# Optimization experiments

Hardware: AMD Instinct MI355X
Metric: run time of the kernel (lower is better)

The kernel has to match this reference:

```python
import jax, jax.numpy as jnp
import numpy as np

EPS = 1e-5

def _layernorm(x, g, b):
    mu = jnp.mean(x, axis=-1, keepdims=True)
    var = jnp.mean(jnp.square(x - mu), axis=-1, keepdims=True)
    return (x - mu) * jax.lax.rsqrt(var + EPS) * g + b

def setup_inputs() -> dict:
    key = jax.random.key(0)
    ks = jax.random.split(key, 5)
    F_, H, D = 1024, 16, 64
    B, N = 4, 2048
    s = lambda k, shp, fan: jax.random.normal(k, shp, jnp.float32) * (fan ** -0.5)
    return {
        "x": jax.random.normal(ks[0], (B, N, F_), jnp.float32),
        "Wq": s(ks[1], (H * D, F_), F_),
        "Wkv": s(ks[2], (2 * H * D, F_), F_),
        "Wo": s(ks[3], (F_, H * D), H * D),
        "ln_g": jnp.ones((F_,), jnp.float32),
        "ln_b": jnp.zeros((F_,), jnp.float32),
        "lnc_g": jnp.ones((F_,), jnp.float32),
        "lnc_b": jnp.zeros((F_,), jnp.float32),
    }

def reference(x, Wq, Wkv, Wo, ln_g, ln_b, lnc_g, lnc_b):
    H, D = 16, 64
    scale = D ** -0.5
    skip = x
    xn = _layernorm(x, ln_g, ln_b)          # query path norm
    cn = _layernorm(x, lnc_g, lnc_b)        # context (self) norm
    B, N, _ = x.shape
    q = jnp.einsum('bnf,ef->bne', xn, Wq)   # [B,N,H*D]
    kv = jnp.einsum('bnf,ef->bne', cn, Wkv) # [B,N,2*H*D]
    k, v = jnp.split(kv, 2, axis=-1)
    tohd = lambda t: t.reshape(B, N, H, D).transpose(0, 2, 1, 3)  # b h n d
    q, k, v = tohd(q), tohd(k), tohd(v)
    sim = jnp.einsum('bhnd,bhmd->bhnm', q, k) * scale
    attn = jax.nn.softmax(sim, axis=-1)
    out = jnp.einsum('bhnm,bhmd->bhnd', attn, v)
    out = out.transpose(0, 2, 1, 3).reshape(B, N, H * D)
    out = jnp.einsum('bne,fe->bnf', out, Wo)
    return skip + out
```

## Files before the change

### kernel.cpp

```cpp
#include <hip/hip_runtime.h>
#include <hip/hip_bf16.h>
#include <stdint.h>

typedef __bf16 bf16;
typedef __bf16 bf16x8 __attribute__((ext_vector_type(8)));
typedef __bf16 bf16x4 __attribute__((ext_vector_type(4)));
typedef float f32x4 __attribute__((ext_vector_type(4)));
typedef unsigned u32x2 __attribute__((ext_vector_type(2)));

#define F_DIM 1024
#define NSEQ  2048
#define NB    4
#define NH    16
#define HD    64
#define MROWS (NB * NSEQ)
#define LOG2E 1.44269504088896340736f

__device__ __forceinline__ void gload_lds16(const void* g, void* l) {
    __builtin_amdgcn_global_load_lds(
        (__attribute__((address_space(1))) void*)g,
        (__attribute__((address_space(3))) void*)l,
        16, 0, 0);
}

__device__ __forceinline__ unsigned lds_addr(const void* p) {
    return (unsigned)(size_t)(__attribute__((address_space(3))) const void*)p;
}

__device__ __forceinline__ float exp2_fast(float x) {
    float r;
    asm("v_exp_f32 %0, %1" : "=v"(r) : "v"(x));
    return r;
}

__device__ __forceinline__ unsigned cvtpk_bf16(float lo, float hi) {
    unsigned r;
    asm("v_cvt_pk_bf16_f32 %0, %1, %2" : "=v"(r) : "v"(lo), "v"(hi));
    return r;
}

__global__ __launch_bounds__(256) void ln2_kernel(
    const float* __restrict__ x,
    const float* __restrict__ g1, const float* __restrict__ b1,
    const float* __restrict__ g2, const float* __restrict__ b2,
    bf16* __restrict__ xn, bf16* __restrict__ cn)
{
    const int row = blockIdx.x;
    const int t = threadIdx.x;
    float4 v = reinterpret_cast<const float4*>(x + (size_t)row * F_DIM)[t];
    float s  = v.x + v.y + v.z + v.w;
    float ss = v.x * v.x + v.y * v.y + v.z * v.z + v.w * v.w;
#pragma unroll
    for (int m = 1; m < 64; m <<= 1) {
        s  += __shfl_xor(s, m);
        ss += __shfl_xor(ss, m);
    }
    __shared__ float red[8];
    const int w = t >> 6;
    if ((t & 63) == 0) { red[w] = s; red[4 + w] = ss; }
    __syncthreads();
    s  = red[0] + red[1] + red[2] + red[3];
    ss = red[4] + red[5] + red[6] + red[7];
    const float mu  = s * (1.0f / F_DIM);
    const float var = fmaxf(ss * (1.0f / F_DIM) - mu * mu, 0.0f);
    const float rs  = rsqrtf(var + 1e-5f);

    float4 G1 = reinterpret_cast<const float4*>(g1)[t];
    float4 B1 = reinterpret_cast<const float4*>(b1)[t];
    float4 G2 = reinterpret_cast<const float4*>(g2)[t];
    float4 B2 = reinterpret_cast<const float4*>(b2)[t];
    const float h0 = (v.x - mu) * rs, h1 = (v.y - mu) * rs;
    const float h2 = (v.z - mu) * rs, h3 = (v.w - mu) * rs;
    bf16x4 o1 = { (bf16)(h0 * G1.x + B1.x), (bf16)(h1 * G1.y + B1.y),
                  (bf16)(h2 * G1.z + B1.z), (bf16)(h3 * G1.w + B1.w) };
    bf16x4 o2 = { (bf16)(h0 * G2.x + B2.x), (bf16)(h1 * G2.y + B2.y),
                  (bf16)(h2 * G2.z + B2.z), (bf16)(h3 * G2.w + B2.w) };
    *reinterpret_cast<bf16x4*>(xn + (size_t)row * F_DIM + t * 4) = o1;
    *reinterpret_cast<bf16x4*>(cn + (size_t)row * F_DIM + t * 4) = o2;
}

__global__ __launch_bounds__(256) void cvt_kernel(
    const float* __restrict__ src, bf16* __restrict__ dst, int n4)
{
    int i = blockIdx.x * 256 + threadIdx.x;
    if (i < n4) {
        float4 v = reinterpret_cast<const float4*>(src)[i];
        bf16x4 o = { (bf16)v.x, (bf16)v.y, (bf16)v.z, (bf16)v.w };
        reinterpret_cast<bf16x4*>(dst)[i] = o;
    }
}

template <int EPI>
__global__ __launch_bounds__(256, 2) void gemm_bt(
    const bf16* __restrict__ A, const bf16* __restrict__ B,
    bf16* __restrict__ Cb, float* __restrict__ Cf,
    const float* __restrict__ skip, int M, int N, int K, float oscale)
{
    __shared__ bf16 As[128 * 32];
    __shared__ bf16 Bs[128 * 32];
    const int t = threadIdx.x;
    const int lane = t & 63;
    const int w = t >> 6;
    const int wr = w >> 1, wc = w & 1;

    int flat = blockIdx.y * gridDim.x + blockIdx.x;
    const int nwg = gridDim.x * gridDim.y;
    if ((nwg & 7) == 0)
        flat = (flat & 7) * (nwg >> 3) + (flat >> 3);
    const int bm = (flat / gridDim.x) * 128;
    const int bn = (flat % gridDim.x) * 128;

    const int r = lane & 15;
    const int kg = (lane >> 4) * 8;

    f32x4 acc[4][4];
#pragma unroll
    for (int i = 0; i < 4; i++)
#pragma unroll
        for (int j = 0; j < 4; j++) acc[i][j] = (f32x4){0.f, 0.f, 0.f, 0.f};

    const int c0 = t, c1 = 256 + t;
    const size_t aoff0 = (size_t)(bm + (c0 >> 2)) * K + (c0 & 3) * 8;
    const size_t aoff1 = (size_t)(bm + (c1 >> 2)) * K + (c1 & 3) * 8;
    const size_t boff0 = (size_t)(bn + (c0 >> 2)) * K + (c0 & 3) * 8;
    const size_t boff1 = (size_t)(bn + (c1 >> 2)) * K + (c1 & 3) * 8;
    bf16* lA0 = As + (size_t)(0 * 256 + w * 64) * 8;
    bf16* lA1 = As + (size_t)(1 * 256 + w * 64) * 8;
    bf16* lB0 = Bs + (size_t)(0 * 256 + w * 64) * 8;
    bf16* lB1 = Bs + (size_t)(1 * 256 + w * 64) * 8;

    for (int kt = 0; kt < K; kt += 32) {
        gload_lds16(A + aoff0 + kt, lA0);
        gload_lds16(A + aoff1 + kt, lA1);
        gload_lds16(B + boff0 + kt, lB0);
        gload_lds16(B + boff1 + kt, lB1);
        __syncthreads();
        bf16x8 af[4], bfr[4];
#pragma unroll
        for (int mi = 0; mi < 4; mi++)
            af[mi] = *(const bf16x8*)(As + (wr * 64 + mi * 16 + r) * 32 + kg);
#pragma unroll
        for (int ni = 0; ni < 4; ni++)
            bfr[ni] = *(const bf16x8*)(Bs + (wc * 64 + ni * 16 + r) * 32 + kg);
#pragma unroll
        for (int mi = 0; mi < 4; mi++)
#pragma unroll
            for (int ni = 0; ni < 4; ni++)
                acc[mi][ni] = __builtin_amdgcn_mfma_f32_16x16x32_bf16(
                    af[mi], bfr[ni], acc[mi][ni], 0, 0, 0);
        __syncthreads();
    }

    const int g = lane >> 4;
#pragma unroll
    for (int mi = 0; mi < 4; mi++) {
#pragma unroll
        for (int ni = 0; ni < 4; ni++) {
            const int col = bn + wc * 64 + ni * 16 + r;
#pragma unroll
            for (int j = 0; j < 4; j++) {
                const int row = bm + wr * 64 + mi * 16 + g * 4 + j;
                const float vv = acc[mi][ni][j];
                if (EPI == 0) {
                    Cb[(size_t)row * N + col] = (bf16)(vv * oscale);
                } else {
                    Cf[(size_t)row * N + col] = vv + skip[(size_t)row * N + col];
                }
            }
        }
    }
}

__global__ __launch_bounds__(512, 4) void attn_kernel(
    const bf16* __restrict__ q, const bf16* __restrict__ kvp,
    bf16* __restrict__ o)
{
    __shared__ __align__(16) bf16 Ks[128 * 64];
    __shared__ __align__(16) bf16 Vs[128 * 64];
    __shared__ __align__(16) bf16 Ps[8][16 * 72];

    const int bid = blockIdx.x;
    const int idx = (bid & 7) * 128 + (bid >> 3);
    const int bh = idx >> 4;
    const int qt = idx & 15;
    const int b = bh >> 4, h = bh & 15;

    const int t = threadIdx.x, lane = t & 63, w = t >> 6;
    const int r = lane & 15, g = lane >> 4;

    const size_t rowq = (size_t)b * NSEQ;

    size_t ksrc[2], vsrc[2];
#pragma unroll
    for (int c = 0; c < 2; c++) {
        const int p = c * 512 + t;
        const int krow = p >> 3;
        const int kcol = (p & 7) ^ (krow & 7);
        ksrc[c] = (size_t)(rowq + krow) * (2 * F_DIM) + h * HD + kcol * 8;
        const int kvb = p >> 5, dblk = (p >> 3) & 3;
        const int kvl = (p & 7) >> 1, d8 = p & 1;
        vsrc[c] = (size_t)(rowq + kvb * 4 + kvl) * (2 * F_DIM) + F_DIM + h * HD
                  + dblk * 16 + d8 * 8;
    }

    const int q0 = qt * 128 + w * 16;
    bf16x8 qf[2];
#pragma unroll
    for (int kk = 0; kk < 2; kk++)
        qf[kk] = *(const bf16x8*)(q + (rowq + q0 + r) * F_DIM + h * HD + kk * 32 + g * 8);

    f32x4 oacc[4];
#pragma unroll
    for (int i = 0; i < 4; i++) oacc[i] = (f32x4){0.f, 0.f, 0.f, 0.f};
    float m_r = -1e30f, l_r = 0.f;

    const unsigned va    = lds_addr(Vs) + (unsigned)(g * 1024 + r * 8);
    const unsigned pbase = lds_addr(&Ps[w][0]) + (unsigned)((r * 72 + g * 8) * 2);

    for (int kv0 = 0; kv0 < NSEQ; kv0 += 128) {
        asm volatile("s_barrier" ::: "memory");
        const size_t koff = (size_t)kv0 * (2 * F_DIM);
#pragma unroll
        for (int c = 0; c < 2; c++) {
            gload_lds16(kvp + ksrc[c] + koff, Ks + (size_t)(c * 512 + (t & ~63)) * 8);
            gload_lds16(kvp + vsrc[c] + koff, Vs + (size_t)(c * 512 + (t & ~63)) * 8);
        }
        asm volatile("s_waitcnt vmcnt(0)\n\ts_barrier" ::: "memory");

        f32x4 s4[8];
#pragma unroll
        for (int nt = 0; nt < 8; nt++) s4[nt] = (f32x4){0.f, 0.f, 0.f, 0.f};
        __builtin_amdgcn_s_setprio(1);
#pragma unroll
        for (int kk = 0; kk < 2; kk++) {
#pragma unroll
            for (int nt = 0; nt < 8; nt++) {
                const unsigned lb = (unsigned)((nt * 16 + r) * 128 + kk * 64 + g * 16)
                                    ^ (unsigned)((r & 7) << 4);
                bf16x8 kf = *(const bf16x8*)((const char*)Ks + lb);
                s4[nt] = __builtin_amdgcn_mfma_f32_16x16x32_bf16(kf, qf[kk], s4[nt], 0, 0, 0);
            }
        }
        __builtin_amdgcn_s_setprio(0);

        float mx = s4[0][0];
#pragma unroll
        for (int nt = 0; nt < 8; nt++)
#pragma unroll
            for (int j = 0; j < 4; j++) mx = fmaxf(mx, s4[nt][j]);
        mx = fmaxf(mx, __shfl_xor(mx, 16));
        mx = fmaxf(mx, __shfl_xor(mx, 32));
        if (!__all(mx <= m_r + 8.0f)) {
            const float mnew = fmaxf(m_r, mx);
            const float alpha = exp2_fast(m_r - mnew);
            l_r *= alpha;
#pragma unroll
            for (int j = 0; j < 4; j++) {
                const float aj = __shfl(alpha, g * 4 + j);
#pragma unroll
                for (int ntd = 0; ntd < 4; ntd++) oacc[ntd][j] *= aj;
            }
            m_r = mnew;
        }
        float ps = 0.f;
#pragma unroll
        for (int nt = 0; nt < 8; nt++)
#pragma unroll
            for (int j = 0; j < 4; j++) {
                const float pp = exp2_fast(s4[nt][j] - m_r);
                s4[nt][j] = pp;
                ps += pp;
            }
        ps += __shfl_xor(ps, 16);
        ps += __shfl_xor(ps, 32);
        l_r += ps;

#pragma unroll
        for (int hh = 0; hh < 2; hh++) {
#pragma unroll
            for (int nt2 = 0; nt2 < 4; nt2++) {
                const int nt = hh * 4 + nt2;
                u32x2 pw = { cvtpk_bf16(s4[nt][0], s4[nt][1]),
                             cvtpk_bf16(s4[nt][2], s4[nt][3]) };
                *(u32x2*)&Ps[w][r * 72 + nt2 * 16 + g * 4] = pw;
            }
            asm volatile("s_waitcnt lgkmcnt(0)" ::: "memory");

            bf16x8 pf[2];
            u32x2 vt[2][4][2];
#pragma unroll
            for (int kk2 = 0; kk2 < 2; kk2++) {
                const unsigned pa = pbase + (unsigned)(kk2 * 64);
                asm volatile("ds_read_b128 %0, %1" : "=v"(pf[kk2]) : "v"(pa));
                const int kkg = hh * 2 + kk2;
#pragma unroll
                for (int ntd = 0; ntd < 4; ntd++) {
                    const unsigned a = va + (unsigned)(kkg * 4096 + ntd * 128);
                    asm volatile("ds_read_b64_tr_b16 %0, %2\n\t"
                                 "ds_read_b64_tr_b16 %1, %2 offset:512"
                                 : "=&v"(vt[kk2][ntd][0]), "=&v"(vt[kk2][ntd][1])
                                 : "v"(a));
                }
            }
            asm volatile("s_waitcnt lgkmcnt(0)" ::: "memory");
            __builtin_amdgcn_sched_barrier(0);

            __builtin_amdgcn_s_setprio(1);
#pragma unroll
            for (int kk2 = 0; kk2 < 2; kk2++)
#pragma unroll
                for (int ntd = 0; ntd < 4; ntd++) {
                    union { u32x2 hl[2]; bf16x8 v; } u;
                    u.hl[0] = vt[kk2][ntd][0];
                    u.hl[1] = vt[kk2][ntd][1];
                    oacc[ntd] = __builtin_amdgcn_mfma_f32_16x16x32_bf16(pf[kk2], u.v, oacc[ntd], 0, 0, 0);
                }
            __builtin_amdgcn_s_setprio(0);
        }
    }

    float rl[4];
#pragma unroll
    for (int j = 0; j < 4; j++) {
        const float lj = __shfl(l_r, g * 4 + j);
        rl[j] = 1.0f / lj;
    }
#pragma unroll
    for (int ntd = 0; ntd < 4; ntd++)
#pragma unroll
        for (int j = 0; j < 4; j++) {
            const int row = q0 + g * 4 + j;
            o[(rowq + row) * F_DIM + h * HD + ntd * 16 + r] =
                (bf16)(oacc[ntd][j] * rl[j]);
        }
}

extern "C" void kernel_launch(void* const* d_in, const int* in_sizes, int n_in,
                              void* d_out, int out_size, void* d_ws, size_t ws_size,
                              hipStream_t stream)
{
    const float* x     = (const float*)d_in[0];
    const float* Wq    = (const float*)d_in[1];
    const float* Wkv   = (const float*)d_in[2];
    const float* Wo    = (const float*)d_in[3];
    const float* ln_g  = (const float*)d_in[4];
    const float* ln_b  = (const float*)d_in[5];
    const float* lnc_g = (const float*)d_in[6];
    const float* lnc_b = (const float*)d_in[7];
    float* out = (float*)d_out;

    bf16* xn   = (bf16*)d_ws;
    bf16* cn   = xn  + (size_t)MROWS * F_DIM;
    bf16* qb   = cn  + (size_t)MROWS * F_DIM;
    bf16* kvb  = qb  + (size_t)MROWS * F_DIM;
    bf16* wqb  = kvb + (size_t)MROWS * 2 * F_DIM;
    bf16* wkvb = wqb + (size_t)F_DIM * F_DIM;
    bf16* wob  = wkvb + (size_t)2 * F_DIM * F_DIM;
    bf16* ao   = xn;

    ln2_kernel<<<dim3(MROWS), dim3(256), 0, stream>>>(x, ln_g, ln_b, lnc_g, lnc_b, xn, cn);

    cvt_kernel<<<dim3((F_DIM * F_DIM / 4 + 255) / 256), dim3(256), 0, stream>>>(Wq, wqb, F_DIM * F_DIM / 4);
    cvt_kernel<<<dim3((2 * F_DIM * F_DIM / 4 + 255) / 256), dim3(256), 0, stream>>>(Wkv, wkvb, 2 * F_DIM * F_DIM / 4);
    cvt_kernel<<<dim3((F_DIM * F_DIM / 4 + 255) / 256), dim3(256), 0, stream>>>(Wo, wob, F_DIM * F_DIM / 4);

    gemm_bt<0><<<dim3(F_DIM / 128, MROWS / 128), dim3(256), 0, stream>>>(
        xn, wqb, qb, nullptr, nullptr, MROWS, F_DIM, F_DIM, 0.125f * LOG2E);
    gemm_bt<0><<<dim3(2 * F_DIM / 128, MROWS / 128), dim3(256), 0, stream>>>(
        cn, wkvb, kvb, nullptr, nullptr, MROWS, 2 * F_DIM, F_DIM, 1.0f);
    attn_kernel<<<dim3(NSEQ / 128 * NB * NH), dim3(512), 0, stream>>>(qb, kvb, ao);
    gemm_bt<1><<<dim3(F_DIM / 128, MROWS / 128), dim3(256), 0, stream>>>(
        ao, wob, nullptr, out, x, MROWS, F_DIM, F_DIM, 1.0f);
}
```

Before: 234.9 us.

## Merge Q and KV projections into one launch and specialize GEMMs

```diff
diff --git a/kernel.cpp b/kernel.cpp
--- a/kernel.cpp
+++ b/kernel.cpp
@@ -90,11 +90,10 @@
     }
 }
 
-template <int EPI>
-__global__ __launch_bounds__(256, 2) void gemm_bt(
-    const bf16* __restrict__ A, const bf16* __restrict__ B,
-    bf16* __restrict__ Cb, float* __restrict__ Cf,
-    const float* __restrict__ skip, int M, int N, int K, float oscale)
+__global__ __launch_bounds__(256, 2) void qkv_gemm(
+    const bf16* __restrict__ xn, const bf16* __restrict__ cn,
+    const bf16* __restrict__ wq, const bf16* __restrict__ wkv,
+    bf16* __restrict__ qb, bf16* __restrict__ kvb, float qscale)
 {
     __shared__ bf16 As[128 * 32];
     __shared__ bf16 Bs[128 * 32];
@@ -103,12 +102,21 @@
     const int w = t >> 6;
     const int wr = w >> 1, wc = w & 1;
 
-    int flat = blockIdx.y * gridDim.x + blockIdx.x;
-    const int nwg = gridDim.x * gridDim.y;
-    if ((nwg & 7) == 0)
-        flat = (flat & 7) * (nwg >> 3) + (flat >> 3);
-    const int bm = (flat / gridDim.x) * 128;
-    const int bn = (flat % gridDim.x) * 128;
+    int flat = blockIdx.x;
+    flat = (flat & 7) * 192 + (flat >> 3);
+
+    const bf16 *A, *B;
+    bf16* C;
+    int N, bm, bn;
+    float osc;
+    if (flat < 512) {
+        A = xn; B = wq; C = qb; N = 1024; osc = qscale;
+        bm = (flat >> 3) * 128; bn = (flat & 7) * 128;
+    } else {
+        const int f = flat - 512;
+        A = cn; B = wkv; C = kvb; N = 2048; osc = 1.0f;
+        bm = (f >> 4) * 128; bn = (f & 15) * 128;
+    }
 
     const int r = lane & 15;
     const int kg = (lane >> 4) * 8;
@@ -120,16 +128,16 @@
         for (int j = 0; j < 4; j++) acc[i][j] = (f32x4){0.f, 0.f, 0.f, 0.f};
 
     const int c0 = t, c1 = 256 + t;
-    const size_t aoff0 = (size_t)(bm + (c0 >> 2)) * K + (c0 & 3) * 8;
-    const size_t aoff1 = (size_t)(bm + (c1 >> 2)) * K + (c1 & 3) * 8;
-    const size_t boff0 = (size_t)(bn + (c0 >> 2)) * K + (c0 & 3) * 8;
-    const size_t boff1 = (size_t)(bn + (c1 >> 2)) * K + (c1 & 3) * 8;
+    const size_t aoff0 = (size_t)(bm + (c0 >> 2)) * F_DIM + (c0 & 3) * 8;
+    const size_t aoff1 = (size_t)(bm + (c1 >> 2)) * F_DIM + (c1 & 3) * 8;
+    const size_t boff0 = (size_t)(bn + (c0 >> 2)) * F_DIM + (c0 & 3) * 8;
+    const size_t boff1 = (size_t)(bn + (c1 >> 2)) * F_DIM + (c1 & 3) * 8;
     bf16* lA0 = As + (size_t)(0 * 256 + w * 64) * 8;
     bf16* lA1 = As + (size_t)(1 * 256 + w * 64) * 8;
     bf16* lB0 = Bs + (size_t)(0 * 256 + w * 64) * 8;
     bf16* lB1 = Bs + (size_t)(1 * 256 + w * 64) * 8;
 
-    for (int kt = 0; kt < K; kt += 32) {
+    for (int kt = 0; kt < F_DIM; kt += 32) {
         gload_lds16(A + aoff0 + kt, lA0);
         gload_lds16(A + aoff1 + kt, lA1);
         gload_lds16(B + boff0 + kt, lB0);
@@ -160,18 +168,88 @@
 #pragma unroll
             for (int j = 0; j < 4; j++) {
                 const int row = bm + wr * 64 + mi * 16 + g * 4 + j;
-                const float vv = acc[mi][ni][j];
-                if (EPI == 0) {
-                    Cb[(size_t)row * N + col] = (bf16)(vv * oscale);
-                } else {
-                    Cf[(size_t)row * N + col] = vv + skip[(size_t)row * N + col];
-                }
+                C[(size_t)row * N + col] = (bf16)(acc[mi][ni][j] * osc);
             }
         }
     }
 }
 
-__global__ __launch_bounds__(512, 4) void attn_kernel(
+__global__ __launch_bounds__(256, 2) void o_gemm(
+    const bf16* __restrict__ A, const bf16* __restrict__ B,
+    float* __restrict__ Cf, const float* __restrict__ skip)
+{
+    __shared__ bf16 As[128 * 32];
+    __shared__ bf16 Bs[128 * 32];
+    const int t = threadIdx.x;
+    const int lane = t & 63;
+    const int w = t >> 6;
+    const int wr = w >> 1, wc = w & 1;
+
+    int flat = blockIdx.x;
+    flat = (flat & 7) * 64 + (flat >> 3);
+    const int bm = (flat >> 3) * 128;
+    const int bn = (flat & 7) * 128;
+
+    const int r = lane & 15;
+    const int kg = (lane >> 4) * 8;
+
+    f32x4 acc[4][4];
+#pragma unroll
+    for (int i = 0; i < 4; i++)
+#pragma unroll
+        for (int j = 0; j < 4; j++) acc[i][j] = (f32x4){0.f, 0.f, 0.f, 0.f};
+
+    const int c0 = t, c1 = 256 + t;
+    const size_t aoff0 = (size_t)(bm + (c0 >> 2)) * F_DIM + (c0 & 3) * 8;
+    const size_t aoff1 = (size_t)(bm + (c1 >> 2)) * F_DIM + (c1 & 3) * 8;
+    const size_t boff0 = (size_t)(bn + (c0 >> 2)) * F_DIM + (c0 & 3) * 8;
+    const size_t boff1 = (size_t)(bn + (c1 >> 2)) * F_DIM + (c1 & 3) * 8;
+    bf16* lA0 = As + (size_t)(0 * 256 + w * 64) * 8;
+    bf16* lA1 = As + (size_t)(1 * 256 + w * 64) * 8;
+    bf16* lB0 = Bs + (size_t)(0 * 256 + w * 64) * 8;
+    bf16* lB1 = Bs + (size_t)(1 * 256 + w * 64) * 8;
+
+    for (int kt = 0; kt < F_DIM; kt += 32) {
+        gload_lds16(A + aoff0 + kt, lA0);
+        gload_lds16(A + aoff1 + kt, lA1);
+        gload_lds16(B + boff0 + kt, lB0);
+        gload_lds16(B + boff1 + kt, lB1);
+        __syncthreads();
+        bf16x8 af[4], bfr[4];
+#pragma unroll
+        for (int mi = 0; mi < 4; mi++)
+            af[mi] = *(const bf16x8*)(As + (wr * 64 + mi * 16 + r) * 32 + kg);
+#pragma unroll
+        for (int ni = 0; ni < 4; ni++)
+            bfr[ni] = *(const bf16x8*)(Bs + (wc * 64 + ni * 16 + r) * 32 + kg);
+#pragma unroll
+        for (int mi = 0; mi < 4; mi++)
+#pragma unroll
+            for (int ni = 0; ni < 4; ni++)
+                acc[mi][ni] = __builtin_amdgcn_mfma_f32_16x16x32_bf16(
+                    af[mi], bfr[ni], acc[mi][ni], 0, 0, 0);
+        __syncthreads();
+    }
+
+    const int g = lane >> 4;
+#pragma unroll
+    for (int mi = 0; mi < 4; mi++) {
+#pragma unroll
+        for (int ni = 0; ni < 4; ni++) {
+            const int col = bn + wc * 64 + ni * 16 + r;
+#pragma unroll
+            for (int j = 0; j < 4; j++) {
+                const int row = bm + wr * 64 + mi * 16 + g * 4 + j;
+                Cf[(size_t)row * F_DIM + col] =
+                    acc[mi][ni][j] + skip[(size_t)row * F_DIM + col];
+            }
+        }
+    }
+}
+
+__global__ __launch_bounds__(512)
+__attribute__((amdgpu_waves_per_eu(4, 5)))
+void attn_kernel(
     const bf16* __restrict__ q, const bf16* __restrict__ kvp,
     bf16* __restrict__ o)
 {
@@ -262,15 +340,17 @@
             }
             m_r = mnew;
         }
+        u32x2 pa2[8];
         float ps = 0.f;
 #pragma unroll
-        for (int nt = 0; nt < 8; nt++)
-#pragma unroll
-            for (int j = 0; j < 4; j++) {
-                const float pp = exp2_fast(s4[nt][j] - m_r);
-                s4[nt][j] = pp;
-                ps += pp;
-            }
+        for (int nt = 0; nt < 8; nt++) {
+            const float e0 = exp2_fast(s4[nt][0] - m_r);
+            const float e1 = exp2_fast(s4[nt][1] - m_r);
+            const float e2 = exp2_fast(s4[nt][2] - m_r);
+            const float e3 = exp2_fast(s4[nt][3] - m_r);
+            ps += (e0 + e1) + (e2 + e3);
+            pa2[nt] = (u32x2){ cvtpk_bf16(e0, e1), cvtpk_bf16(e2, e3) };
+        }
         ps += __shfl_xor(ps, 16);
         ps += __shfl_xor(ps, 32);
         l_r += ps;
@@ -278,12 +358,8 @@
 #pragma unroll
         for (int hh = 0; hh < 2; hh++) {
 #pragma unroll
-            for (int nt2 = 0; nt2 < 4; nt2++) {
-                const int nt = hh * 4 + nt2;
-                u32x2 pw = { cvtpk_bf16(s4[nt][0], s4[nt][1]),
-                             cvtpk_bf16(s4[nt][2], s4[nt][3]) };
-                *(u32x2*)&Ps[w][r * 72 + nt2 * 16 + g * 4] = pw;
-            }
+            for (int nt2 = 0; nt2 < 4; nt2++)
+                *(u32x2*)&Ps[w][r * 72 + nt2 * 16 + g * 4] = pa2[hh * 4 + nt2];
             asm volatile("s_waitcnt lgkmcnt(0)" ::: "memory");
 
             bf16x8 pf[2];
@@ -364,11 +440,8 @@
     cvt_kernel<<<dim3((2 * F_DIM * F_DIM / 4 + 255) / 256), dim3(256), 0, stream>>>(Wkv, wkvb, 2 * F_DIM * F_DIM / 4);
     cvt_kernel<<<dim3((F_DIM * F_DIM / 4 + 255) / 256), dim3(256), 0, stream>>>(Wo, wob, F_DIM * F_DIM / 4);
 
-    gemm_bt<0><<<dim3(F_DIM / 128, MROWS / 128), dim3(256), 0, stream>>>(
-        xn, wqb, qb, nullptr, nullptr, MROWS, F_DIM, F_DIM, 0.125f * LOG2E);
-    gemm_bt<0><<<dim3(2 * F_DIM / 128, MROWS / 128), dim3(256), 0, stream>>>(
-        cn, wkvb, kvb, nullptr, nullptr, MROWS, 2 * F_DIM, F_DIM, 1.0f);
+    qkv_gemm<<<dim3(1536), dim3(256), 0, stream>>>(
+        xn, cn, wqb, wkvb, qb, kvb, 0.125f * LOG2E);
     attn_kernel<<<dim3(NSEQ / 128 * NB * NH), dim3(512), 0, stream>>>(qb, kvb, ao);
-    gemm_bt<1><<<dim3(F_DIM / 128, MROWS / 128), dim3(256), 0, stream>>>(
-        ao, wob, nullptr, out, x, MROWS, F_DIM, F_DIM, 1.0f);
-}
+    o_gemm<<<dim3(512), dim3(256), 0, stream>>>(ao, wob, out, x);
+}
```

Result: faster. 219.7 us (-6.5%).
